# Kernel tuning notes

Hardware: AMD Instinct MI355X
Metric: run time of the kernel (lower is better)

## Reference

```python
import jax, jax.numpy as jnp
import numpy as np

EMBED_DIM = 1024
NUM_HEADS = 16
HEAD_DIM = EMBED_DIM // NUM_HEADS


def setup_inputs() -> dict:
    key = jax.random.key(0)
    ks = jax.random.split(key, 6)
    B, S, E = 2, 2048, EMBED_DIM
    sd = 1.0 / np.sqrt(E)
    return {
        "x": jax.random.normal(ks[0], (B, S, E), dtype=jnp.float32),
        "attention_mask": jnp.zeros((B, S, S), dtype=jnp.float32),
        "in_proj_weight": jax.random.normal(ks[1], (3 * E, E), dtype=jnp.float32) * sd,
        "in_proj_bias": jax.random.normal(ks[2], (3 * E,), dtype=jnp.float32) * 0.02,
        "out_proj_weight": jax.random.normal(ks[3], (E, E), dtype=jnp.float32) * sd,
        "out_proj_bias": jax.random.normal(ks[4], (E,), dtype=jnp.float32) * 0.02,
    }


def reference(x, attention_mask, in_proj_weight, in_proj_bias, out_proj_weight, out_proj_bias):
    B, S, E = x.shape
    H, D = NUM_HEADS, HEAD_DIM
    # fused QKV projection: [B,S,3E]
    qkv = jnp.einsum('bse,fe->bsf', x, in_proj_weight) + in_proj_bias
    q, k, v = jnp.split(qkv, 3, axis=-1)
    # [B,S,E] -> [B,H,S,D]
    def to_heads(t):
        return t.reshape(B, S, H, D).transpose(0, 2, 1, 3)
    q, k, v = to_heads(q), to_heads(k), to_heads(v)
    scale = jnp.sqrt(jnp.asarray(D, dtype=x.dtype))
    p = jnp.einsum('bhsd,bhtd->bhst', q / scale, k)  # [B,H,S,S]
    p = p + attention_mask[:, None, :, :] * (-10000.0)
    a = jax.nn.softmax(p, axis=-1)
    # dropout p=0.0 / eval mode: identity
    y = jnp.einsum('bhst,bhtd->bhsd', a, v)  # [B,H,S,D]
    y = y.transpose(0, 2, 1, 3).reshape(B, S, E)
    return jnp.einsum('bse,fe->bsf', y, out_proj_weight) + out_proj_bias
```

## Files before the change

kernel.cpp:

```cpp
#include <hip/hip_runtime.h>
#include <cstdint>
#include <cstddef>

#define S_LEN 2048
#define EMB   1024
#define NH    16
#define HD    64
#define E3    3072

typedef __attribute__((ext_vector_type(8))) short b16x8;
typedef __attribute__((ext_vector_type(4))) float f32x4;

__device__ __forceinline__ ushort bf16_rne(float f) {
    uint32_t u = __float_as_uint(f);
    uint32_t r = (u + 0x7FFFu + ((u >> 16) & 1u)) >> 16;
    return (ushort)r;
}
__device__ __forceinline__ void split2(float f, ushort* h, ushort* l) {
    ushort hh = bf16_rne(f);
    *h = hh;
    float rem = f - __uint_as_float(((uint32_t)hh) << 16);
    *l = bf16_rne(rem);
}

__global__ __launch_bounds__(256) void split_f32_kernel(
    const float4* __restrict__ src, ushort4* __restrict__ h,
    ushort4* __restrict__ l, int n4)
{
    int i = blockIdx.x * 256 + threadIdx.x;
    if (i >= n4) return;
    float4 v = src[i];
    ushort4 hv, lv;
    split2(v.x, &hv.x, &lv.x);
    split2(v.y, &hv.y, &lv.y);
    split2(v.z, &hv.z, &lv.z);
    split2(v.w, &hv.w, &lv.w);
    h[i] = hv; l[i] = lv;
}

__device__ __forceinline__ void gload16(const void* g, void* lds) {
    __builtin_amdgcn_global_load_lds(
        (const __attribute__((address_space(1))) uint32_t*)g,
        (__attribute__((address_space(3))) uint32_t*)lds, 16, 0, 0);
}

__global__ __launch_bounds__(256, 2) void gemm_qkv(
    const ushort* __restrict__ Ah, const ushort* __restrict__ Al,
    const ushort* __restrict__ Bh, const ushort* __restrict__ Bl,
    const float* __restrict__ bias,
    ushort* __restrict__ qkvh, ushort* __restrict__ qkvl,
    ushort* __restrict__ Vth, ushort* __restrict__ Vtl)
{
    const int K = 1024;
    __shared__ __align__(16) ushort ldsT[4][128 * 64];

    const int t    = threadIdx.x;
    const int lane = t & 63;
    const int wave = t >> 6;
    const int wm   = wave >> 1, wn = wave & 1;
    const int bm0  = blockIdx.y * 128, bn0 = blockIdx.x * 128;

    f32x4 acc[4][4];
#pragma unroll
    for (int i = 0; i < 4; ++i)
#pragma unroll
        for (int j = 0; j < 4; ++j) acc[i][j] = (f32x4){0.f, 0.f, 0.f, 0.f};

    for (int k0 = 0; k0 < K; k0 += 64) {
        __syncthreads();
#pragma unroll
        for (int rep = 0; rep < 16; ++rep) {
            const int tile = rep >> 2;
            const int sig  = (rep & 3) * 256 + t;
            const int row  = sig >> 3;
            const int slot = sig & 7;
            const int slog = slot ^ (row & 7);
            const ushort* src = (tile == 0) ? Ah : (tile == 1) ? Al
                              : (tile == 2) ? Bh : Bl;
            const int rb = (tile < 2) ? bm0 : bn0;
            gload16(src + (size_t)(rb + row) * K + k0 + slog * 8,
                    &ldsT[tile][sig * 8]);
        }
        __syncthreads();

#pragma unroll
        for (int s = 0; s < 2; ++s) {
            b16x8 af[4][2], bf[4][2];
#pragma unroll
            for (int i = 0; i < 4; ++i) {
                const int rA = wm * 64 + i * 16 + (lane & 15);
                const int sA = (s * 4 + (lane >> 4)) ^ (rA & 7);
                af[i][0] = *(const b16x8*)&ldsT[0][rA * 64 + sA * 8];
                af[i][1] = *(const b16x8*)&ldsT[1][rA * 64 + sA * 8];
                const int rB = wn * 64 + i * 16 + (lane & 15);
                const int sB = (s * 4 + (lane >> 4)) ^ (rB & 7);
                bf[i][0] = *(const b16x8*)&ldsT[2][rB * 64 + sB * 8];
                bf[i][1] = *(const b16x8*)&ldsT[3][rB * 64 + sB * 8];
            }
#pragma unroll
            for (int i = 0; i < 4; ++i)
#pragma unroll
                for (int j = 0; j < 4; ++j) {
                    acc[i][j] = __builtin_amdgcn_mfma_f32_16x16x32_bf16(
                        af[i][0], bf[j][0], acc[i][j], 0, 0, 0);
                    acc[i][j] = __builtin_amdgcn_mfma_f32_16x16x32_bf16(
                        af[i][0], bf[j][1], acc[i][j], 0, 0, 0);
                    acc[i][j] = __builtin_amdgcn_mfma_f32_16x16x32_bf16(
                        af[i][1], bf[j][0], acc[i][j], 0, 0, 0);
                }
        }
    }

#pragma unroll
    for (int i = 0; i < 4; ++i) {
        const int row = bm0 + wm * 64 + i * 16 + (lane >> 4) * 4;
#pragma unroll
        for (int j = 0; j < 4; ++j) {
            const int col = bn0 + wn * 64 + j * 16 + (lane & 15);
            const float bv = bias[col];
            if (col < 2048) {
                const float sc = (col < 1024) ? 0.125f : 1.0f;
#pragma unroll
                for (int r = 0; r < 4; ++r) {
                    float v = (acc[i][j][r] + bv) * sc;
                    ushort hh, ll;
                    split2(v, &hh, &ll);
                    qkvh[(size_t)(row + r) * 2048 + col] = hh;
                    qkvl[(size_t)(row + r) * 2048 + col] = ll;
                }
            } else {
                const int d = (col - 2048) & 63, hh_ = (col - 2048) >> 6;
                const int b = row >> 11, s = row & 2047;
                ushort4 hv, lv;
                float v0 = acc[i][j][0] + bv, v1 = acc[i][j][1] + bv;
                float v2 = acc[i][j][2] + bv, v3 = acc[i][j][3] + bv;
                split2(v0, &hv.x, &lv.x);
                split2(v1, &hv.y, &lv.y);
                split2(v2, &hv.z, &lv.z);
                split2(v3, &hv.w, &lv.w);
                size_t off = ((size_t)(b * NH + hh_) * 64 + d) * S_LEN + s;
                *(ushort4*)(Vth + off) = hv;
                *(ushort4*)(Vtl + off) = lv;
            }
        }
    }
}

__global__ __launch_bounds__(256, 2) void gemm_split_bf16(
    const ushort* __restrict__ Ah, const ushort* __restrict__ Al,
    const ushort* __restrict__ Bh, const ushort* __restrict__ Bl,
    const float* __restrict__ bias, float* __restrict__ C,
    int M, int N, int K)
{
    __shared__ __align__(16) ushort ldsT[4][128 * 64];

    const int t    = threadIdx.x;
    const int lane = t & 63;
    const int wave = t >> 6;
    const int wm   = wave >> 1, wn = wave & 1;
    const int bm0  = blockIdx.y * 128, bn0 = blockIdx.x * 128;

    f32x4 acc[4][4];
#pragma unroll
    for (int i = 0; i < 4; ++i)
#pragma unroll
        for (int j = 0; j < 4; ++j) acc[i][j] = (f32x4){0.f, 0.f, 0.f, 0.f};

    for (int k0 = 0; k0 < K; k0 += 64) {
        __syncthreads();
#pragma unroll
        for (int rep = 0; rep < 16; ++rep) {
            const int tile = rep >> 2;
            const int sig  = (rep & 3) * 256 + t;
            const int row  = sig >> 3;
            const int slot = sig & 7;
            const int slog = slot ^ (row & 7);
            const ushort* src = (tile == 0) ? Ah : (tile == 1) ? Al
                              : (tile == 2) ? Bh : Bl;
            const int rb = (tile < 2) ? bm0 : bn0;
            gload16(src + (size_t)(rb + row) * K + k0 + slog * 8,
                    &ldsT[tile][sig * 8]);
        }
        __syncthreads();

#pragma unroll
        for (int s = 0; s < 2; ++s) {
            b16x8 af[4][2], bf[4][2];
#pragma unroll
            for (int i = 0; i < 4; ++i) {
                const int rA = wm * 64 + i * 16 + (lane & 15);
                const int sA = (s * 4 + (lane >> 4)) ^ (rA & 7);
                af[i][0] = *(const b16x8*)&ldsT[0][rA * 64 + sA * 8];
                af[i][1] = *(const b16x8*)&ldsT[1][rA * 64 + sA * 8];
                const int rB = wn * 64 + i * 16 + (lane & 15);
                const int sB = (s * 4 + (lane >> 4)) ^ (rB & 7);
                bf[i][0] = *(const b16x8*)&ldsT[2][rB * 64 + sB * 8];
                bf[i][1] = *(const b16x8*)&ldsT[3][rB * 64 + sB * 8];
            }
#pragma unroll
            for (int i = 0; i < 4; ++i)
#pragma unroll
                for (int j = 0; j < 4; ++j) {
                    acc[i][j] = __builtin_amdgcn_mfma_f32_16x16x32_bf16(
                        af[i][0], bf[j][0], acc[i][j], 0, 0, 0);
                    acc[i][j] = __builtin_amdgcn_mfma_f32_16x16x32_bf16(
                        af[i][0], bf[j][1], acc[i][j], 0, 0, 0);
                    acc[i][j] = __builtin_amdgcn_mfma_f32_16x16x32_bf16(
                        af[i][1], bf[j][0], acc[i][j], 0, 0, 0);
                }
        }
    }

#pragma unroll
    for (int i = 0; i < 4; ++i) {
        const int row = bm0 + wm * 64 + i * 16 + (lane >> 4) * 4;
#pragma unroll
        for (int j = 0; j < 4; ++j) {
            const int col = bn0 + wn * 64 + j * 16 + (lane & 15);
            const float bv = bias[col];
#pragma unroll
            for (int r = 0; r < 4; ++r)
                C[(size_t)(row + r) * N + col] = acc[i][j][r] + bv;
        }
    }
}

__global__ __launch_bounds__(256, 3) void attn_mfma(
    const ushort* __restrict__ qkvh, const ushort* __restrict__ qkvl,
    const ushort* __restrict__ Vth, const ushort* __restrict__ Vtl,
    const float* __restrict__ mask,
    ushort* __restrict__ Yh, ushort* __restrict__ Yl)
{
    __shared__ __align__(16) ushort KV[4][4096];
    __shared__ __align__(16) ushort Qs[2][4096];
    ushort* Ps = &Qs[0][0];

    const int t    = threadIdx.x;
    const int lane = t & 63;
    const int w    = t >> 6;
    const int l15  = lane & 15;
    const int lg   = lane >> 4;
    const int qb   = blockIdx.x;
    const int bh   = blockIdx.y;
    const int b    = bh >> 4, h = bh & 15;

#pragma unroll
    for (int c = 0; c < 4; ++c) {
        int idx = c * 256 + t;
        int buf = idx >> 9, ci = idx & 511, row = ci >> 3, slot = ci & 7;
        const ushort* src = (buf ? qkvl : qkvh)
            + (size_t)(b * S_LEN + qb * 64 + row) * 2048 + h * 64
            + (slot ^ (row & 7)) * 8;
        gload16(src, &Qs[buf][ci * 8]);
    }
    __syncthreads();

    b16x8 qf[2][2];
    {
        const int qrow = w * 16 + l15;
        const int sw   = qrow & 7;
#pragma unroll
        for (int ks = 0; ks < 2; ++ks) {
            qf[ks][0] = *(const b16x8*)&Qs[0][qrow * 64 + (((ks * 4 + lg) ^ sw) * 8)];
            qf[ks][1] = *(const b16x8*)&Qs[1][qrow * 64 + (((ks * 4 + lg) ^ sw) * 8)];
        }
    }
    __syncthreads();

    float m_run = -3.0e38f, l_run = 0.0f;
    f32x4 accO[4];
#pragma unroll
    for (int fi = 0; fi < 4; ++fi) accO[fi] = (f32x4){0.f, 0.f, 0.f, 0.f};

    const float* Mrow = mask + (size_t)b * S_LEN * S_LEN
                      + (size_t)(qb * 64 + w * 16 + l15) * S_LEN;
    const int prow = w * 16 + l15;
    const int psw  = prow & 7;

    for (int kv0 = 0; kv0 < S_LEN; kv0 += 64) {
        __syncthreads();
#pragma unroll
        for (int c = 0; c < 8; ++c) {
            int idx = c * 256 + t;
            int sel = idx >> 9, ci = idx & 511, row = ci >> 3, slot = ci & 7;
            int sc = (slot ^ (row & 7)) * 8;
            const ushort* src;
            if (sel == 0)
                src = qkvh + (size_t)(b * S_LEN + kv0 + row) * 2048 + 1024 + h * 64 + sc;
            else if (sel == 1)
                src = qkvl + (size_t)(b * S_LEN + kv0 + row) * 2048 + 1024 + h * 64 + sc;
            else if (sel == 2)
                src = Vth + (size_t)((b * NH + h) * 64 + row) * S_LEN + kv0 + sc;
            else
                src = Vtl + (size_t)((b * NH + h) * 64 + row) * S_LEN + kv0 + sc;
            gload16(src, &KV[sel][ci * 8]);
        }
        __syncthreads();

        f32x4 c4[4];
#pragma unroll
        for (int fi = 0; fi < 4; ++fi) {
            float4 mv = *(const float4*)(Mrow + kv0 + fi * 16 + lg * 4);
            c4[fi][0] = mv.x * -10000.f;
            c4[fi][1] = mv.y * -10000.f;
            c4[fi][2] = mv.z * -10000.f;
            c4[fi][3] = mv.w * -10000.f;
        }
#pragma unroll
        for (int fi = 0; fi < 4; ++fi) {
            const int krow = fi * 16 + l15;
            const int sw   = krow & 7;
            b16x8 kh0 = *(const b16x8*)&KV[0][krow * 64 + (((0 + lg) ^ sw) * 8)];
            b16x8 kh1 = *(const b16x8*)&KV[0][krow * 64 + (((4 + lg) ^ sw) * 8)];
            b16x8 kl0 = *(const b16x8*)&KV[1][krow * 64 + (((0 + lg) ^ sw) * 8)];
            b16x8 kl1 = *(const b16x8*)&KV[1][krow * 64 + (((4 + lg) ^ sw) * 8)];
            c4[fi] = __builtin_amdgcn_mfma_f32_16x16x32_bf16(kh0, qf[0][0], c4[fi], 0, 0, 0);
            c4[fi] = __builtin_amdgcn_mfma_f32_16x16x32_bf16(kh0, qf[0][1], c4[fi], 0, 0, 0);
            c4[fi] = __builtin_amdgcn_mfma_f32_16x16x32_bf16(kl0, qf[0][0], c4[fi], 0, 0, 0);
            c4[fi] = __builtin_amdgcn_mfma_f32_16x16x32_bf16(kh1, qf[1][0], c4[fi], 0, 0, 0);
            c4[fi] = __builtin_amdgcn_mfma_f32_16x16x32_bf16(kh1, qf[1][1], c4[fi], 0, 0, 0);
            c4[fi] = __builtin_amdgcn_mfma_f32_16x16x32_bf16(kl1, qf[1][0], c4[fi], 0, 0, 0);
        }

        float mt = fmaxf(fmaxf(fmaxf(c4[0][0], c4[0][1]), fmaxf(c4[0][2], c4[0][3])),
                         fmaxf(fmaxf(c4[1][0], c4[1][1]), fmaxf(c4[1][2], c4[1][3])));
        mt = fmaxf(mt, fmaxf(fmaxf(fmaxf(c4[2][0], c4[2][1]), fmaxf(c4[2][2], c4[2][3])),
                             fmaxf(fmaxf(c4[3][0], c4[3][1]), fmaxf(c4[3][2], c4[3][3]))));
        mt = fmaxf(mt, __shfl_xor(mt, 16));
        mt = fmaxf(mt, __shfl_xor(mt, 32));
        const float mn   = fmaxf(m_run, mt);
        const float corr = __expf(m_run - mn);
        float p[4][4];
        float ps = 0.f;
#pragma unroll
        for (int fi = 0; fi < 4; ++fi)
#pragma unroll
            for (int r = 0; r < 4; ++r) {
                p[fi][r] = __expf(c4[fi][r] - mn);
                ps += p[fi][r];
            }
        ps += __shfl_xor(ps, 16);
        ps += __shfl_xor(ps, 32);
        l_run = l_run * corr + ps;
        m_run = mn;

#pragma unroll
        for (int fi = 0; fi < 4; ++fi) {
            const int kvb  = fi * 16 + lg * 4;
            const int slot = kvb >> 3;
            ushort4 pv;
            pv.x = bf16_rne(p[fi][0]);
            pv.y = bf16_rne(p[fi][1]);
            pv.z = bf16_rne(p[fi][2]);
            pv.w = bf16_rne(p[fi][3]);
            *(ushort4*)&Ps[prow * 64 + ((slot ^ psw) * 16) / 2 + (kvb & 7)] = pv;
        }

        float cr0 = __shfl(corr, lg * 4 + 0);
        float cr1 = __shfl(corr, lg * 4 + 1);
        float cr2 = __shfl(corr, lg * 4 + 2);
        float cr3 = __shfl(corr, lg * 4 + 3);
#pragma unroll
        for (int fi = 0; fi < 4; ++fi) {
            accO[fi][0] *= cr0; accO[fi][1] *= cr1;
            accO[fi][2] *= cr2; accO[fi][3] *= cr3;
        }

        b16x8 pf0 = *(const b16x8*)&Ps[prow * 64 + (((0 + lg) ^ psw) * 8)];
        b16x8 pf1 = *(const b16x8*)&Ps[prow * 64 + (((4 + lg) ^ psw) * 8)];
#pragma unroll
        for (int fi = 0; fi < 4; ++fi) {
            const int vrow = fi * 16 + l15;
            const int sw   = vrow & 7;
            b16x8 vh0 = *(const b16x8*)&KV[2][vrow * 64 + (((0 + lg) ^ sw) * 8)];
            b16x8 vh1 = *(const b16x8*)&KV[2][vrow * 64 + (((4 + lg) ^ sw) * 8)];
            b16x8 vl0 = *(const b16x8*)&KV[3][vrow * 64 + (((0 + lg) ^ sw) * 8)];
            b16x8 vl1 = *(const b16x8*)&KV[3][vrow * 64 + (((4 + lg) ^ sw) * 8)];
            accO[fi] = __builtin_amdgcn_mfma_f32_16x16x32_bf16(pf0, vh0, accO[fi], 0, 0, 0);
            accO[fi] = __builtin_amdgcn_mfma_f32_16x16x32_bf16(pf0, vl0, accO[fi], 0, 0, 0);
            accO[fi] = __builtin_amdgcn_mfma_f32_16x16x32_bf16(pf1, vh1, accO[fi], 0, 0, 0);
            accO[fi] = __builtin_amdgcn_mfma_f32_16x16x32_bf16(pf1, vl1, accO[fi], 0, 0, 0);
        }
    }

    const float il = 1.0f / l_run;
    float ir[4];
    ir[0] = __shfl(il, lg * 4 + 0);
    ir[1] = __shfl(il, lg * 4 + 1);
    ir[2] = __shfl(il, lg * 4 + 2);
    ir[3] = __shfl(il, lg * 4 + 3);
#pragma unroll
    for (int fi = 0; fi < 4; ++fi)
#pragma unroll
        for (int r = 0; r < 4; ++r) {
            float y = accO[fi][r] * ir[r];
            ushort hy, ly;
            split2(y, &hy, &ly);
            size_t off = (size_t)(b * S_LEN + qb * 64 + w * 16 + lg * 4 + r) * EMB
                       + h * 64 + fi * 16 + l15;
            Yh[off] = hy;
            Yl[off] = ly;
        }
}

extern "C" void kernel_launch(void* const* d_in, const int* in_sizes, int n_in,
                              void* d_out, int out_size, void* d_ws, size_t ws_size,
                              hipStream_t stream)
{
    const float* x     = (const float*)d_in[0];
    const float* mask  = (const float*)d_in[1];
    const float* w_in  = (const float*)d_in[2];
    const float* b_in  = (const float*)d_in[3];
    const float* w_out = (const float*)d_in[4];
    const float* b_out = (const float*)d_in[5];
    float* out = (float*)d_out;

    char* ws = (char*)d_ws;
    ushort* qkvh = (ushort*)(ws + 0);
    ushort* qkvl = (ushort*)(ws + 16777216);
    ushort* Vth  = (ushort*)(ws + 33554432);
    ushort* Vtl  = (ushort*)(ws + 41943040);
    ushort* Xh   = (ushort*)(ws + 50331648);
    ushort* Xl   = (ushort*)(ws + 58720256);
    ushort* Wih  = (ushort*)(ws + 67108864);
    ushort* Wil  = (ushort*)(ws + 73400320);
    ushort* Woh  = (ushort*)(ws + 79691776);
    ushort* Wol  = (ushort*)(ws + 81788928);
    ushort* Yh = Xh;
    ushort* Yl = Xl;

    split_f32_kernel<<<4096, 256, 0, stream>>>((const float4*)x,
        (ushort4*)Xh, (ushort4*)Xl, 1048576);
    split_f32_kernel<<<3072, 256, 0, stream>>>((const float4*)w_in,
        (ushort4*)Wih, (ushort4*)Wil, 786432);
    split_f32_kernel<<<1024, 256, 0, stream>>>((const float4*)w_out,
        (ushort4*)Woh, (ushort4*)Wol, 262144);

    gemm_qkv<<<dim3(E3 / 128, 4096 / 128), 256, 0, stream>>>(
        Xh, Xl, Wih, Wil, b_in, qkvh, qkvl, Vth, Vtl);

    attn_mfma<<<dim3(S_LEN / 64, 2 * NH), 256, 0, stream>>>(
        qkvh, qkvl, Vth, Vtl, mask, Yh, Yl);

    gemm_split_bf16<<<dim3(EMB / 128, 4096 / 128), 256, 0, stream>>>(
        Yh, Yl, Woh, Wol, b_out, out, 4096, EMB, EMB);
}
```

Before: 392.0 us.

## Double-buffer KV tiles and prefetch mask in attention loop, remap block order

Turns the attention inner loop into a double-buffered pipeline: the next K/V tile is staged into a second LDS buffer and the next mask slice is loaded into registers while the current tile is computed, leaving one barrier per iteration instead of two. The block index is also remapped so that concurrently scheduled blocks spread across batch/head pairs, which may change L2 locality. LDS use roughly doubles for the KV buffers and launch bounds drop to 2 waves per SIMD, which lowers occupancy. The Ps scratch region aliases Qs, so correctness depends on barrier placement within the unseen softmax section.

New measurement: 385.5 us. Within noise of the previous version (-1.7%).

```diff
diff --git a/kernel.cpp b/kernel.cpp
--- a/kernel.cpp
+++ b/kernel.cpp
@@ -225,13 +225,36 @@
     }
 }
 
-__global__ __launch_bounds__(256, 3) void attn_mfma(
+__device__ __forceinline__ void stage_kv_tile(
+    const ushort* __restrict__ qkvh, const ushort* __restrict__ qkvl,
+    const ushort* __restrict__ Vth, const ushort* __restrict__ Vtl,
+    int b, int h, int kv0, int t, ushort* dst )
+{
+#pragma unroll
+    for (int c = 0; c < 8; ++c) {
+        int idx = c * 256 + t;
+        int sel = idx >> 9, ci = idx & 511, row = ci >> 3, slot = ci & 7;
+        int sc = (slot ^ (row & 7)) * 8;
+        const ushort* src;
+        if (sel == 0)
+            src = qkvh + (size_t)(b * S_LEN + kv0 + row) * 2048 + 1024 + h * 64 + sc;
+        else if (sel == 1)
+            src = qkvl + (size_t)(b * S_LEN + kv0 + row) * 2048 + 1024 + h * 64 + sc;
+        else if (sel == 2)
+            src = Vth + (size_t)((b * NH + h) * 64 + row) * S_LEN + kv0 + sc;
+        else
+            src = Vtl + (size_t)((b * NH + h) * 64 + row) * S_LEN + kv0 + sc;
+        gload16(src, dst + sel * 4096 + ci * 8);
+    }
+}
+
+__global__ __launch_bounds__(256, 2) void attn_mfma(
     const ushort* __restrict__ qkvh, const ushort* __restrict__ qkvl,
     const ushort* __restrict__ Vth, const ushort* __restrict__ Vtl,
     const float* __restrict__ mask,
     ushort* __restrict__ Yh, ushort* __restrict__ Yl)
 {
-    __shared__ __align__(16) ushort KV[4][4096];
+    __shared__ __align__(16) ushort KVb[2][4][4096];
     __shared__ __align__(16) ushort Qs[2][4096];
     ushort* Ps = &Qs[0][0];
 
@@ -240,9 +263,11 @@
     const int w    = t >> 6;
     const int l15  = lane & 15;
     const int lg   = lane >> 4;
-    const int qb   = blockIdx.x;
-    const int bh   = blockIdx.y;
-    const int b    = bh >> 4, h = bh & 15;
+
+    const int d  = blockIdx.y * 32 + blockIdx.x;
+    const int wy = 4 * (d & 7) + ((d >> 3) >> 5);
+    const int qb = (d >> 3) & 31;
+    const int b  = wy >> 4, h = wy & 15;
 
 #pragma unroll
     for (int c = 0; c < 4; ++c) {
@@ -253,6 +278,15 @@
             + (slot ^ (row & 7)) * 8;
         gload16(src, &Qs[buf][ci * 8]);
     }
+    stage_kv_tile(qkvh, qkvl, Vth, Vtl, b, h, 0, t, &KVb[0][0][0]);
+
+    const float* Mrow = mask + (size_t)b * S_LEN * S_LEN
+                      + (size_t)(qb * 64 + w * 16 + l15) * S_LEN;
+    float4 mcur[4], mnext[4];
+#pragma unroll
+    for (int fi = 0; fi < 4; ++fi)
+        mcur[fi] = *(const float4*)(Mrow + fi * 16 + lg * 4);
+
     __syncthreads();
 
     b16x8 qf[2][2];
@@ -272,48 +306,40 @@
 #pragma unroll
     for (int fi = 0; fi < 4; ++fi) accO[fi] = (f32x4){0.f, 0.f, 0.f, 0.f};
 
-    const float* Mrow = mask + (size_t)b * S_LEN * S_LEN
-                      + (size_t)(qb * 64 + w * 16 + l15) * S_LEN;
     const int prow = w * 16 + l15;
     const int psw  = prow & 7;
 
+    int buf = 0;
     for (int kv0 = 0; kv0 < S_LEN; kv0 += 64) {
-        __syncthreads();
-#pragma unroll
-        for (int c = 0; c < 8; ++c) {
-            int idx = c * 256 + t;
-            int sel = idx >> 9, ci = idx & 511, row = ci >> 3, slot = ci & 7;
-            int sc = (slot ^ (row & 7)) * 8;
-            const ushort* src;
-            if (sel == 0)
-                src = qkvh + (size_t)(b * S_LEN + kv0 + row) * 2048 + 1024 + h * 64 + sc;
-            else if (sel == 1)
-                src = qkvl + (size_t)(b * S_LEN + kv0 + row) * 2048 + 1024 + h * 64 + sc;
-            else if (sel == 2)
-                src = Vth + (size_t)((b * NH + h) * 64 + row) * S_LEN + kv0 + sc;
-            else
-                src = Vtl + (size_t)((b * NH + h) * 64 + row) * S_LEN + kv0 + sc;
-            gload16(src, &KV[sel][ci * 8]);
-        }
-        __syncthreads();
+        const bool notlast = (kv0 + 64 < S_LEN);
+        if (notlast) {
+            stage_kv_tile(qkvh, qkvl, Vth, Vtl, b, h, kv0 + 64, t,
+                          &KVb[buf ^ 1][0][0]);
+#pragma unroll
+            for (int fi = 0; fi < 4; ++fi)
+                mnext[fi] = *(const float4*)(Mrow + kv0 + 64 + fi * 16 + lg * 4);
+        }
+        const ushort* Kh = &KVb[buf][0][0];
+        const ushort* Kl = &KVb[buf][1][0];
+        const ushort* Vh = &KVb[buf][2][0];
+        const ushort* Vl = &KVb[buf][3][0];
 
         f32x4 c4[4];
 #pragma unroll
         for (int fi = 0; fi < 4; ++fi) {
-            float4 mv = *(const float4*)(Mrow + kv0 + fi * 16 + lg * 4);
-            c4[fi][0] = mv.x * -10000.f;
-            c4[fi][1] = mv.y * -10000.f;
-            c4[fi][2] = mv.z * -10000.f;
-            c4[fi][3] = mv.w * -10000.f;
+            c4[fi][0] = mcur[fi].x * -10000.f;
+            c4[fi][1] = mcur[fi].y * -10000.f;
+            c4[fi][2] = mcur[fi].z * -10000.f;
+            c4[fi][3] = mcur[fi].w * -10000.f;
         }
 #pragma unroll
         for (int fi = 0; fi < 4; ++fi) {
             const int krow = fi * 16 + l15;
             const int sw   = krow & 7;
-            b16x8 kh0 = *(const b16x8*)&KV[0][krow * 64 + (((0 + lg) ^ sw) * 8)];
-            b16x8 kh1 = *(const b16x8*)&KV[0][krow * 64 + (((4 + lg) ^ sw) * 8)];
-            b16x8 kl0 = *(const b16x8*)&KV[1][krow * 64 + (((0 + lg) ^ sw) * 8)];
-            b16x8 kl1 = *(const b16x8*)&KV[1][krow * 64 + (((4 + lg) ^ sw) * 8)];
+            b16x8 kh0 = *(const b16x8*)&Kh[krow * 64 + (((0 + lg) ^ sw) * 8)];
+            b16x8 kh1 = *(const b16x8*)&Kh[krow * 64 + (((4 + lg) ^ sw) * 8)];
+            b16x8 kl0 = *(const b16x8*)&Kl[krow * 64 + (((0 + lg) ^ sw) * 8)];
+            b16x8 kl1 = *(const b16x8*)&Kl[krow * 64 + (((4 + lg) ^ sw) * 8)];
             c4[fi] = __builtin_amdgcn_mfma_f32_16x16x32_bf16(kh0, qf[0][0], c4[fi], 0, 0, 0);
             c4[fi] = __builtin_amdgcn_mfma_f32_16x16x32_bf16(kh0, qf[0][1], c4[fi], 0, 0, 0);
             c4[fi] = __builtin_amdgcn_mfma_f32_16x16x32_bf16(kl0, qf[0][0], c4[fi], 0, 0, 0);
@@ -372,15 +398,23 @@
         for (int fi = 0; fi < 4; ++fi) {
             const int vrow = fi * 16 + l15;
             const int sw   = vrow & 7;
-            b16x8 vh0 = *(const b16x8*)&KV[2][vrow * 64 + (((0 + lg) ^ sw) * 8)];
-            b16x8 vh1 = *(const b16x8*)&KV[2][vrow * 64 + (((4 + lg) ^ sw) * 8)];
-            b16x8 vl0 = *(const b16x8*)&KV[3][vrow * 64 + (((0 + lg) ^ sw) * 8)];
-            b16x8 vl1 = *(const b16x8*)&KV[3][vrow * 64 + (((4 + lg) ^ sw) * 8)];
+            b16x8 vh0 = *(const b16x8*)&Vh[vrow * 64 + (((0 + lg) ^ sw) * 8)];
+            b16x8 vh1 = *(const b16x8*)&Vh[vrow * 64 + (((4 + lg) ^ sw) * 8)];
+            b16x8 vl0 = *(const b16x8*)&Vl[vrow * 64 + (((0 + lg) ^ sw) * 8)];
+            b16x8 vl1 = *(const b16x8*)&Vl[vrow * 64 + (((4 + lg) ^ sw) * 8)];
             accO[fi] = __builtin_amdgcn_mfma_f32_16x16x32_bf16(pf0, vh0, accO[fi], 0, 0, 0);
             accO[fi] = __builtin_amdgcn_mfma_f32_16x16x32_bf16(pf0, vl0, accO[fi], 0, 0, 0);
             accO[fi] = __builtin_amdgcn_mfma_f32_16x16x32_bf16(pf1, vh1, accO[fi], 0, 0, 0);
             accO[fi] = __builtin_amdgcn_mfma_f32_16x16x32_bf16(pf1, vl1, accO[fi], 0, 0, 0);
         }
+
+        if (notlast) {
+#pragma unroll
+            for (int fi = 0; fi < 4; ++fi) mcur[fi] = mnext[fi];
+        }
+
+        __syncthreads();
+        buf ^= 1;
     }
 
     const float il = 1.0f / l_run;
```
